# Kernel optimization log

Measured on AMD Instinct MI355X. Metric: run time of the kernel, lower is better.

## Reference

```python
import jax, jax.numpy as jnp
import numpy as np

DIM_MODEL = 512
DIM_HEAD = 64


def setup_inputs() -> dict:
    key = jax.random.key(0)
    ks = jax.random.split(key, 7)
    B, S = 4, 4096
    scale = 1.0 / np.sqrt(DIM_MODEL)
    x = jax.random.normal(ks[0], (B, S, DIM_MODEL), dtype=jnp.float32)
    # nn.Linear weights: stored as [out, in] in torch; we use [in, out] for x @ W
    Wq = jax.random.uniform(ks[1], (DIM_MODEL, DIM_HEAD), jnp.float32, -scale, scale)
    Wk = jax.random.uniform(ks[2], (DIM_MODEL, DIM_HEAD), jnp.float32, -scale, scale)
    Wv = jax.random.uniform(ks[3], (DIM_MODEL, DIM_HEAD), jnp.float32, -scale, scale)
    bq = jax.random.uniform(ks[4], (DIM_HEAD,), jnp.float32, -scale, scale)
    bk = jax.random.uniform(ks[5], (DIM_HEAD,), jnp.float32, -scale, scale)
    bv = jax.random.uniform(ks[6], (DIM_HEAD,), jnp.float32, -scale, scale)
    return {"x": x, "Wq": Wq, "bq": bq, "Wk": Wk, "bk": bk, "Wv": Wv, "bv": bv}


def reference(x, Wq, bq, Wk, bk, Wv, bv):
    # [q,k,v] = z @ U_qkv
    q = x @ Wq + bq  # [B, S, Dh]
    k = x @ Wk + bk
    v = x @ Wv + bv
    dot_scale = jnp.sqrt(jnp.asarray(DIM_HEAD, dtype=x.dtype))
    scores = jnp.einsum("bsd,btd->bst", q, k) / dot_scale  # [B, S, S]
    attn = jax.nn.softmax(scores, axis=-1)
    return jnp.einsum("bst,btd->bsd", attn, v)  # [B, S, Dh]
```

## Files before the change

### kernel.cpp

```cpp
#include <hip/hip_runtime.h>
#include <hip/hip_bf16.h>

typedef short short8 __attribute__((ext_vector_type(8)));
typedef float f32x4 __attribute__((ext_vector_type(4)));

#define MFMA16(a,b,c) __builtin_amdgcn_mfma_f32_16x16x32_bf16((a),(b),(c),0,0,0)

#define NROWS 16384
#define LOG2E 1.44269504088896340736f

#define OFF_Q  0u
#define OFF_K  (2u<<20)
#define OFF_V  (4u<<20)
#define OFF_W  (6u<<20)
#define OFF_O  ((6u<<20) + (1u<<18))

__device__ __forceinline__ unsigned short f2bf(float f){
    union { float f; unsigned u; } v; v.f = f;
    unsigned r = v.u + 0x7FFFu + ((v.u >> 16) & 1u);
    return (unsigned short)(r >> 16);
}
__device__ __forceinline__ unsigned pk2(float a, float b){
    union { __hip_bfloat162 h; unsigned u; } c;
    c.h = __float22bfloat162_rn(make_float2(a, b));
    return c.u;
}

union Frag {
    short8 s;
    unsigned short u[8];
    uint2 d2[2];
    uint4 q4;
};

__global__ __launch_bounds__(256) void wprep_kernel(
    const float* __restrict__ Wq, const float* __restrict__ Wk,
    const float* __restrict__ Wv, unsigned short* __restrict__ wfrag)
{
    int idx = blockIdx.x * 256 + threadIdx.x;
    int lane = idx & 63;
    int rest = idx >> 6;
    int kk = rest & 15;
    int nt = (rest >> 4) & 3;
    int w  = rest >> 6;
    const float* W = (w == 0) ? Wq : (w == 1) ? Wk : Wv;
    float scl = (w == 0) ? (0.125f * LOG2E) : 1.0f;
    int n = 16 * nt + (lane & 15);
    int g = lane >> 4;
    Frag o;
#pragma unroll
    for (int e = 0; e < 8; ++e) {
        int k = 32 * kk + 16 * (e >> 2) + 4 * g + (e & 3);
        o.u[e] = f2bf(W[k * 64 + n] * scl);
    }
    *(uint4*)(wfrag + (size_t)idx * 8) = o.q4;
}

#define LDW(WD, KK) do { \
    _Pragma("unroll") \
    for (int nt_ = 0; nt_ < 4; ++nt_) \
        WD[nt_].q4 = wf[((size_t)(nt_ * 16 + (KK))) * 64 + lane]; \
    } while (0)

#define DOK(WC, KK) do { \
    Frag xf_; \
    xf_.d2[0] = *(const uint2*)&xs[l15][32 * (KK) + 4 * g]; \
    xf_.d2[1] = *(const uint2*)&xs[l15][32 * (KK) + 16 + 4 * g]; \
    if (w == 2) { \
        _Pragma("unroll") \
        for (int nt_ = 0; nt_ < 4; ++nt_) acc[nt_] = MFMA16(xf_.s, WC[nt_].s, acc[nt_]); \
    } else { \
        _Pragma("unroll") \
        for (int nt_ = 0; nt_ < 4; ++nt_) acc[nt_] = MFMA16(WC[nt_].s, xf_.s, acc[nt_]); \
    } } while (0)

__global__ __launch_bounds__(192) void qkv_kernel(
    const float* __restrict__ x,
    const float* __restrict__ bq, const float* __restrict__ bk,
    const float* __restrict__ bv,
    const unsigned short* __restrict__ wfrag,
    unsigned short* __restrict__ qfrag,
    unsigned short* __restrict__ kfrag,
    unsigned short* __restrict__ vfrag)
{
    __shared__ unsigned short xs[16][520];
    const int tid = threadIdx.x;
    const int lane = tid & 63;
    const int w = tid >> 6;
    const int l15 = lane & 15, g = lane >> 4;
    const int rg = blockIdx.x;
    const float* xbase = x + (size_t)rg * 16 * 512;

    for (int i = tid; i < 2048; i += 192) {
        float4 v = *(const float4*)(xbase + i * 4);
        int r_ = i >> 7;
        int c_ = (i & 127) * 4;
        *(uint2*)&xs[r_][c_] = make_uint2(pk2(v.x, v.y), pk2(v.z, v.w));
    }
    __syncthreads();

    f32x4 acc[4];
#pragma unroll
    for (int nt = 0; nt < 4; ++nt) acc[nt] = (f32x4){0.f,0.f,0.f,0.f};

    const uint4* wf = (const uint4*)wfrag + (size_t)w * 4096;

    Frag wA[4], wB[4];
    LDW(wA, 0);
#pragma unroll
    for (int kp = 0; kp < 8; ++kp) {
        LDW(wB, 2 * kp + 1);
        __builtin_amdgcn_sched_barrier(0);
        DOK(wA, 2 * kp);
        if (2 * kp + 2 < 16) LDW(wA, 2 * kp + 2);
        __builtin_amdgcn_sched_barrier(0);
        DOK(wB, 2 * kp + 1);
    }

    const int b   = rg >> 8;
    const int rgb = rg & 255;
    const int tc  = rgb >> 2;
    const int c   = rgb & 3;

    if (w == 0) {
#pragma unroll
        for (int nt = 0; nt < 4; ++nt) {
            float4 bb = *(const float4*)(bq + 16 * nt + 4 * g);
            const float bs = 0.125f * LOG2E;
            float q0 = acc[nt][0] + bb.x * bs;
            float q1 = acc[nt][1] + bb.y * bs;
            float q2 = acc[nt][2] + bb.z * bs;
            float q3 = acc[nt][3] + bb.w * bs;
            int ks = nt >> 1, h = nt & 1;
            size_t qoff = ((size_t)(rg * 2 + ks) * 64 + lane) * 8 + h * 4;
            *(uint2*)(qfrag + qoff) = make_uint2(pk2(q0, q1), pk2(q2, q3));
        }
    } else if (w == 1) {
#pragma unroll
        for (int nt = 0; nt < 4; ++nt) {
            float4 bb = *(const float4*)(bk + 16 * nt + 4 * g);
            float k0 = acc[nt][0] + bb.x;
            float k1 = acc[nt][1] + bb.y;
            float k2 = acc[nt][2] + bb.z;
            float k3 = acc[nt][3] + bb.w;
            int ks = nt >> 1, h = nt & 1;
            size_t kfi = ((size_t)((b * 64 + tc) * 4 + c) * 2 + ks);
            size_t koff = (kfi * 64 + lane) * 8 + h * 4;
            *(uint2*)(kfrag + koff) = make_uint2(pk2(k0, k1), pk2(k2, k3));
        }
    } else {
        const int vks = c >> 1, vh = c & 1;
#pragma unroll
        for (int nt = 0; nt < 4; ++nt) {
            float bvv = bv[16 * nt + l15];
            float v0 = acc[nt][0] + bvv;
            float v1 = acc[nt][1] + bvv;
            float v2 = acc[nt][2] + bvv;
            float v3 = acc[nt][3] + bvv;
            size_t vfi = ((size_t)((b * 64 + tc) * 4 + nt) * 2 + vks);
            size_t voff = (vfi * 64 + lane) * 8 + vh * 4;
            *(uint2*)(vfrag + voff) = make_uint2(pk2(v0, v1), pk2(v2, v3));
        }
    }
}

#define LOADK(KD, CH) do { \
    const uint4* p_ = kb0 + (size_t)(CH) * 512; \
    _Pragma("unroll") \
    for (int c_ = 0; c_ < 4; ++c_) { \
        KD[c_][0].q4 = p_[(c_ * 2 + 0) * 64]; \
        KD[c_][1].q4 = p_[(c_ * 2 + 1) * 64]; \
    } } while (0)

#define LOADV(VD, CH) do { \
    const uint4* p_ = vb0 + (size_t)(CH) * 512; \
    _Pragma("unroll") \
    for (int c_ = 0; c_ < 4; ++c_) { \
        VD[c_][0].q4 = p_[(c_ * 2 + 0) * 64]; \
        VD[c_][1].q4 = p_[(c_ * 2 + 1) * 64]; \
    } } while (0)

#define BODY(KC, KN, CH, CHN) do { \
    Frag vC[4][2]; \
    LOADV(vC, CH); \
    LOADK(KN, CHN); \
    __builtin_amdgcn_sched_barrier(0); \
    _Pragma("unroll") \
    for (int M_ = 0; M_ < 4; ++M_) { \
        f32x4 sD[4]; \
        __builtin_amdgcn_s_setprio(1); \
        _Pragma("unroll") \
        for (int c_ = 0; c_ < 4; ++c_) { \
            f32x4 D = (f32x4){0.f,0.f,0.f,0.f}; \
            D = MFMA16(KC[c_][0].s, qf[M_][0].s, D); \
            D = MFMA16(KC[c_][1].s, qf[M_][1].s, D); \
            sD[c_] = D; \
        } \
        __builtin_amdgcn_s_setprio(0); \
        Frag pa0, pa1; \
        _Pragma("unroll") \
        for (int c_ = 0; c_ < 4; ++c_) { \
            float p0 = __builtin_exp2f(sD[c_][0]); \
            float p1 = __builtin_exp2f(sD[c_][1]); \
            float p2 = __builtin_exp2f(sD[c_][2]); \
            float p3 = __builtin_exp2f(sD[c_][3]); \
            uint2 pk_ = make_uint2(pk2(p0, p1), pk2(p2, p3)); \
            if (c_ < 2) pa0.d2[c_ & 1] = pk_; else pa1.d2[c_ & 1] = pk_; \
        } \
        __builtin_amdgcn_s_setprio(1); \
        lacc[M_] = MFMA16(pa0.s, ones_.s, lacc[M_]); \
        lacc[M_] = MFMA16(pa1.s, ones_.s, lacc[M_]); \
        _Pragma("unroll") \
        for (int dc_ = 0; dc_ < 4; ++dc_) { \
            acc[M_][dc_] = MFMA16(pa0.s, vC[dc_][0].s, acc[M_][dc_]); \
            acc[M_][dc_] = MFMA16(pa1.s, vC[dc_][1].s, acc[M_][dc_]); \
        } \
        __builtin_amdgcn_s_setprio(0); \
    } } while (0)

__global__ __launch_bounds__(256, 2) void attn_kernel(
    const unsigned short* __restrict__ qfrag,
    const unsigned short* __restrict__ kfrag,
    const unsigned short* __restrict__ vfrag,
    uint2* __restrict__ OpartU, float* __restrict__ lml,
    int CPS, int SBITS)
{
    const int tid = threadIdx.x;
    const int lane = tid & 63;
    const int w = tid >> 6;
    const int l15 = lane & 15, g = lane >> 4;
    const int split  = blockIdx.x & ((1 << SBITS) - 1);
    const int qblock = blockIdx.x >> SBITS;
    const int gw = qblock * 4 + w;
    const int b = gw >> 6;
    const int tcg0 = b * 64 + split * CPS;

    const uint4* qf4 = (const uint4*)qfrag;
    const uint4* kb0 = (const uint4*)kfrag + (size_t)tcg0 * 512 + lane;
    const uint4* vb0 = (const uint4*)vfrag + (size_t)tcg0 * 512 + lane;

    Frag qf[4][2];
#pragma unroll
    for (int M = 0; M < 4; ++M)
#pragma unroll
        for (int ks = 0; ks < 2; ++ks)
            qf[M][ks].q4 = qf4[((size_t)((gw * 4 + M) * 2 + ks)) * 64 + lane];

    Frag ones_;
    ones_.d2[0] = make_uint2(0x3F803F80u, 0x3F803F80u);
    ones_.d2[1] = make_uint2(0x3F803F80u, 0x3F803F80u);

    f32x4 acc[4][4], lacc[4];
#pragma unroll
    for (int M = 0; M < 4; ++M) {
        lacc[M] = (f32x4){0.f,0.f,0.f,0.f};
#pragma unroll
        for (int dc = 0; dc < 4; ++dc) acc[M][dc] = (f32x4){0.f,0.f,0.f,0.f};
    }

    Frag kA[4][2], kB[4][2];
    LOADK(kA, 0);

#pragma unroll 1
    for (int ch = 0; ch < CPS; ch += 2) {
        int c1 = (ch + 1 < CPS) ? (ch + 1) : ch;
        int c2 = (ch + 2 < CPS) ? (ch + 2) : ch;
        BODY(kA, kB, ch, c1);
        BODY(kB, kA, c1, c2);
    }

#pragma unroll
    for (int M = 0; M < 4; ++M) {
#pragma unroll
        for (int dc = 0; dc < 4; ++dc)
            OpartU[((size_t)(split * 256 + gw) * 16 + M * 4 + dc) * 64 + lane] =
                make_uint2(pk2(acc[M][dc][0], acc[M][dc][1]),
                           pk2(acc[M][dc][2], acc[M][dc][3]));
        if (l15 == 0)
            *(f32x4*)(lml + (size_t)(split * 256 + gw) * 64 + M * 16 + 4 * g) = lacc[M];
    }
}

__global__ __launch_bounds__(256) void merge_kernel(
    const uint2* __restrict__ OpartU, const float* __restrict__ lml,
    float* __restrict__ out, int S)
{
    int gid = blockIdx.x * 256 + threadIdx.x;
    int lane = gid & 63;
    int dc = (gid >> 6) & 3;
    int M  = (gid >> 8) & 3;
    int gw = gid >> 10;
    int l15 = lane & 15, g = lane >> 4;

    float o0 = 0.f, o1 = 0.f, o2 = 0.f, o3 = 0.f;
    float L0 = 0.f, L1 = 0.f, L2 = 0.f, L3 = 0.f;
    for (int s = 0; s < S; ++s) {
        uint2 pv = OpartU[((size_t)(s * 256 + gw) * 16 + M * 4 + dc) * 64 + lane];
        float4 lv = *(const float4*)(lml + (size_t)(s * 256 + gw) * 64 + M * 16 + 4 * g);
        o0 += __uint_as_float(pv.x << 16);
        o1 += __uint_as_float(pv.x & 0xFFFF0000u);
        o2 += __uint_as_float(pv.y << 16);
        o3 += __uint_as_float(pv.y & 0xFFFF0000u);
        L0 += lv.x; L1 += lv.y; L2 += lv.z; L3 += lv.w;
    }
    size_t row = (size_t)gw * 64 + M * 16 + 4 * g;
    int col = 16 * dc + l15;
    out[(row + 0) * 64 + col] = o0 / L0;
    out[(row + 1) * 64 + col] = o1 / L1;
    out[(row + 2) * 64 + col] = o2 / L2;
    out[(row + 3) * 64 + col] = o3 / L3;
}

extern "C" void kernel_launch(void* const* d_in, const int* in_sizes, int n_in,
                              void* d_out, int out_size, void* d_ws, size_t ws_size,
                              hipStream_t stream) {
    (void)in_sizes; (void)n_in; (void)out_size;
    const float* x  = (const float*)d_in[0];
    const float* Wq = (const float*)d_in[1];
    const float* bq = (const float*)d_in[2];
    const float* Wk = (const float*)d_in[3];
    const float* bk = (const float*)d_in[4];
    const float* Wv = (const float*)d_in[5];
    const float* bv = (const float*)d_in[6];
    float* out = (float*)d_out;

    char* ws = (char*)d_ws;
    unsigned short* qfrag = (unsigned short*)(ws + OFF_Q);
    unsigned short* kfrag = (unsigned short*)(ws + OFF_K);
    unsigned short* vfrag = (unsigned short*)(ws + OFF_V);
    unsigned short* wfrag = (unsigned short*)(ws + OFF_W);

    const size_t oneO = (size_t)256 * 16 * 64 * 8;
    const size_t oneL = (size_t)256 * 64 * 4;
    int S = 8, SBITS = 3;
    if (ws_size < (size_t)OFF_O + 8 * (oneO + oneL)) { S = 4; SBITS = 2; }
    if (ws_size < (size_t)OFF_O + 4 * (oneO + oneL)) { S = 2; SBITS = 1; }
    uint2* OpartU = (uint2*)(ws + OFF_O);
    float* lml    = (float*)(ws + OFF_O + (size_t)S * oneO);
    int CPS = 64 / S;

    hipLaunchKernelGGL(wprep_kernel, dim3(48), dim3(256), 0, stream,
                       Wq, Wk, Wv, wfrag);
    hipLaunchKernelGGL(qkv_kernel, dim3(1024), dim3(192), 0, stream,
                       x, bq, bk, bv, wfrag, qfrag, kfrag, vfrag);
    hipLaunchKernelGGL(attn_kernel, dim3(64 * S), dim3(256), 0, stream,
                       qfrag, kfrag, vfrag, OpartU, lml, CPS, SBITS);
    hipLaunchKernelGGL(merge_kernel, dim3(1024), dim3(256), 0, stream,
                       OpartU, lml, out, S);
}
```

Before: 59.17 us.

## Fuse split-K merge into attention kernel via shared-memory atomic reduction

The attention kernel now runs 8 waves per block, one per key-chunk split, all for the same 64-query group. Their partial outputs and row sums are combined with shared-memory atomics, and the normalized result is written straight to the output. This removes the bf16 partial-output round trip through global memory and the separate merge kernel launch. In exchange there are LDS atomic contention, two block barriers, a larger block size that may limit occupancy, a fixed split of 8 and a remapped block-to-query order.

```diff
diff --git a/kernel.cpp b/kernel.cpp
--- a/kernel.cpp
+++ b/kernel.cpp
@@ -13,7 +13,6 @@
 #define OFF_K  (2u<<20)
 #define OFF_V  (4u<<20)
 #define OFF_W  (6u<<20)
-#define OFF_O  ((6u<<20) + (1u<<18))
 
 __device__ __forceinline__ unsigned short f2bf(float f){
     union { float f; unsigned u; } v; v.f = f;
@@ -218,22 +217,25 @@
         __builtin_amdgcn_s_setprio(0); \
     } } while (0)
 
-__global__ __launch_bounds__(256, 2) void attn_kernel(
+__global__ __launch_bounds__(512, 2) void attn_kernel(
     const unsigned short* __restrict__ qfrag,
     const unsigned short* __restrict__ kfrag,
     const unsigned short* __restrict__ vfrag,
-    uint2* __restrict__ OpartU, float* __restrict__ lml,
-    int CPS, int SBITS)
+    float* __restrict__ out)
 {
+    __shared__ float Osh[64][65];
+    __shared__ float lsh[64];
     const int tid = threadIdx.x;
     const int lane = tid & 63;
     const int w = tid >> 6;
     const int l15 = lane & 15, g = lane >> 4;
-    const int split  = blockIdx.x & ((1 << SBITS) - 1);
-    const int qblock = blockIdx.x >> SBITS;
-    const int gw = qblock * 4 + w;
+    const int bid = blockIdx.x;
+    const int gw = ((bid & 7) << 5) | (bid >> 3);
     const int b = gw >> 6;
-    const int tcg0 = b * 64 + split * CPS;
+    const int tcg0 = b * 64 + w * 8;
+
+    for (int i = tid; i < 64 * 65; i += 512) (&Osh[0][0])[i] = 0.f;
+    if (tid < 64) lsh[tid] = 0.f;
 
     const uint4* qf4 = (const uint4*)qfrag;
     const uint4* kb0 = (const uint4*)kfrag + (size_t)tcg0 * 512 + lane;
@@ -262,59 +264,40 @@
     LOADK(kA, 0);
 
 #pragma unroll 1
-    for (int ch = 0; ch < CPS; ch += 2) {
-        int c1 = (ch + 1 < CPS) ? (ch + 1) : ch;
-        int c2 = (ch + 2 < CPS) ? (ch + 2) : ch;
+    for (int ch = 0; ch < 8; ch += 2) {
+        int c1 = ch + 1;
+        int c2 = (ch + 2 < 8) ? (ch + 2) : c1;
         BODY(kA, kB, ch, c1);
         BODY(kB, kA, c1, c2);
     }
 
+    __syncthreads();
 #pragma unroll
     for (int M = 0; M < 4; ++M) {
 #pragma unroll
         for (int dc = 0; dc < 4; ++dc)
-            OpartU[((size_t)(split * 256 + gw) * 16 + M * 4 + dc) * 64 + lane] =
-                make_uint2(pk2(acc[M][dc][0], acc[M][dc][1]),
-                           pk2(acc[M][dc][2], acc[M][dc][3]));
-        if (l15 == 0)
-            *(f32x4*)(lml + (size_t)(split * 256 + gw) * 64 + M * 16 + 4 * g) = lacc[M];
-    }
-}
-
-__global__ __launch_bounds__(256) void merge_kernel(
-    const uint2* __restrict__ OpartU, const float* __restrict__ lml,
-    float* __restrict__ out, int S)
-{
-    int gid = blockIdx.x * 256 + threadIdx.x;
-    int lane = gid & 63;
-    int dc = (gid >> 6) & 3;
-    int M  = (gid >> 8) & 3;
-    int gw = gid >> 10;
-    int l15 = lane & 15, g = lane >> 4;
-
-    float o0 = 0.f, o1 = 0.f, o2 = 0.f, o3 = 0.f;
-    float L0 = 0.f, L1 = 0.f, L2 = 0.f, L3 = 0.f;
-    for (int s = 0; s < S; ++s) {
-        uint2 pv = OpartU[((size_t)(s * 256 + gw) * 16 + M * 4 + dc) * 64 + lane];
-        float4 lv = *(const float4*)(lml + (size_t)(s * 256 + gw) * 64 + M * 16 + 4 * g);
-        o0 += __uint_as_float(pv.x << 16);
-        o1 += __uint_as_float(pv.x & 0xFFFF0000u);
-        o2 += __uint_as_float(pv.y << 16);
-        o3 += __uint_as_float(pv.y & 0xFFFF0000u);
-        L0 += lv.x; L1 += lv.y; L2 += lv.z; L3 += lv.w;
-    }
-    size_t row = (size_t)gw * 64 + M * 16 + 4 * g;
-    int col = 16 * dc + l15;
-    out[(row + 0) * 64 + col] = o0 / L0;
-    out[(row + 1) * 64 + col] = o1 / L1;
-    out[(row + 2) * 64 + col] = o2 / L2;
-    out[(row + 3) * 64 + col] = o3 / L3;
+#pragma unroll
+            for (int r = 0; r < 4; ++r)
+                atomicAdd(&Osh[16 * M + 4 * g + r][16 * dc + l15], acc[M][dc][r]);
+        if (l15 == 0) {
+#pragma unroll
+            for (int r = 0; r < 4; ++r)
+                atomicAdd(&lsh[16 * M + 4 * g + r], lacc[M][r]);
+        }
+    }
+    __syncthreads();
+
+    float* outb = out + (size_t)gw * 64 * 64;
+    for (int i = tid; i < 4096; i += 512) {
+        int row = i >> 6, col = i & 63;
+        outb[i] = Osh[row][col] / lsh[row];
+    }
 }
 
 extern "C" void kernel_launch(void* const* d_in, const int* in_sizes, int n_in,
                               void* d_out, int out_size, void* d_ws, size_t ws_size,
                               hipStream_t stream) {
-    (void)in_sizes; (void)n_in; (void)out_size;
+    (void)in_sizes; (void)n_in; (void)out_size; (void)ws_size;
     const float* x  = (const float*)d_in[0];
     const float* Wq = (const float*)d_in[1];
     const float* bq = (const float*)d_in[2];
@@ -330,21 +313,10 @@
     unsigned short* vfrag = (unsigned short*)(ws + OFF_V);
     unsigned short* wfrag = (unsigned short*)(ws + OFF_W);
 
-    const size_t oneO = (size_t)256 * 16 * 64 * 8;
-    const size_t oneL = (size_t)256 * 64 * 4;
-    int S = 8, SBITS = 3;
-    if (ws_size < (size_t)OFF_O + 8 * (oneO + oneL)) { S = 4; SBITS = 2; }
-    if (ws_size < (size_t)OFF_O + 4 * (oneO + oneL)) { S = 2; SBITS = 1; }
-    uint2* OpartU = (uint2*)(ws + OFF_O);
-    float* lml    = (float*)(ws + OFF_O + (size_t)S * oneO);
-    int CPS = 64 / S;
-
     hipLaunchKernelGGL(wprep_kernel, dim3(48), dim3(256), 0, stream,
                        Wq, Wk, Wv, wfrag);
     hipLaunchKernelGGL(qkv_kernel, dim3(1024), dim3(192), 0, stream,
                        x, bq, bk, bv, wfrag, qfrag, kfrag, vfrag);
-    hipLaunchKernelGGL(attn_kernel, dim3(64 * S), dim3(256), 0, stream,
-                       qfrag, kfrag, vfrag, OpartU, lml, CPS, SBITS);
-    hipLaunchKernelGGL(merge_kernel, dim3(1024), dim3(256), 0, stream,
-                       OpartU, lml, out, S);
-}
+    hipLaunchKernelGGL(attn_kernel, dim3(256), dim3(512), 0, stream,
+                       qfrag, kfrag, vfrag, out);
+}
```

After: 91.97 us. 1.55x slower.

## Stage K/V chunks into shared LDS via async global_load_lds double buffering

Applied to the files above, without the earlier changes.

Instead of each wave loading its own K and V fragments from global memory into registers, the four waves of a block cooperatively copy each K/V chunk into a double-buffered LDS tile with global_load_lds, then read the fragments from LDS. This removes the four-fold redundant global/L2 traffic across waves sharing the same batch and frees registers used for K/V prefetch. In exchange it adds LDS reads per MFMA group and a block-wide barrier per chunk. Correctness of the async copy relies on the barrier covering the in-flight global_load_lds, with no explicit vmcnt wait.

```diff
diff --git a/kernel.cpp b/kernel.cpp
--- a/kernel.cpp
+++ b/kernel.cpp
@@ -164,60 +164,6 @@
     }
 }
 
-#define LOADK(KD, CH) do { \
-    const uint4* p_ = kb0 + (size_t)(CH) * 512; \
-    _Pragma("unroll") \
-    for (int c_ = 0; c_ < 4; ++c_) { \
-        KD[c_][0].q4 = p_[(c_ * 2 + 0) * 64]; \
-        KD[c_][1].q4 = p_[(c_ * 2 + 1) * 64]; \
-    } } while (0)
-
-#define LOADV(VD, CH) do { \
-    const uint4* p_ = vb0 + (size_t)(CH) * 512; \
-    _Pragma("unroll") \
-    for (int c_ = 0; c_ < 4; ++c_) { \
-        VD[c_][0].q4 = p_[(c_ * 2 + 0) * 64]; \
-        VD[c_][1].q4 = p_[(c_ * 2 + 1) * 64]; \
-    } } while (0)
-
-#define BODY(KC, KN, CH, CHN) do { \
-    Frag vC[4][2]; \
-    LOADV(vC, CH); \
-    LOADK(KN, CHN); \
-    __builtin_amdgcn_sched_barrier(0); \
-    _Pragma("unroll") \
-    for (int M_ = 0; M_ < 4; ++M_) { \
-        f32x4 sD[4]; \
-        __builtin_amdgcn_s_setprio(1); \
-        _Pragma("unroll") \
-        for (int c_ = 0; c_ < 4; ++c_) { \
-            f32x4 D = (f32x4){0.f,0.f,0.f,0.f}; \
-            D = MFMA16(KC[c_][0].s, qf[M_][0].s, D); \
-            D = MFMA16(KC[c_][1].s, qf[M_][1].s, D); \
-            sD[c_] = D; \
-        } \
-        __builtin_amdgcn_s_setprio(0); \
-        Frag pa0, pa1; \
-        _Pragma("unroll") \
-        for (int c_ = 0; c_ < 4; ++c_) { \
-            float p0 = __builtin_exp2f(sD[c_][0]); \
-            float p1 = __builtin_exp2f(sD[c_][1]); \
-            float p2 = __builtin_exp2f(sD[c_][2]); \
-            float p3 = __builtin_exp2f(sD[c_][3]); \
-            uint2 pk_ = make_uint2(pk2(p0, p1), pk2(p2, p3)); \
-            if (c_ < 2) pa0.d2[c_ & 1] = pk_; else pa1.d2[c_ & 1] = pk_; \
-        } \
-        __builtin_amdgcn_s_setprio(1); \
-        lacc[M_] = MFMA16(pa0.s, ones_.s, lacc[M_]); \
-        lacc[M_] = MFMA16(pa1.s, ones_.s, lacc[M_]); \
-        _Pragma("unroll") \
-        for (int dc_ = 0; dc_ < 4; ++dc_) { \
-            acc[M_][dc_] = MFMA16(pa0.s, vC[dc_][0].s, acc[M_][dc_]); \
-            acc[M_][dc_] = MFMA16(pa1.s, vC[dc_][1].s, acc[M_][dc_]); \
-        } \
-        __builtin_amdgcn_s_setprio(0); \
-    } } while (0)
-
 __global__ __launch_bounds__(256, 2) void attn_kernel(
     const unsigned short* __restrict__ qfrag,
     const unsigned short* __restrict__ kfrag,
@@ -225,6 +171,7 @@
     uint2* __restrict__ OpartU, float* __restrict__ lml,
     int CPS, int SBITS)
 {
+    __shared__ unsigned short lds[2][16][64][8];
     const int tid = threadIdx.x;
     const int lane = tid & 63;
     const int w = tid >> 6;
@@ -236,8 +183,20 @@
     const int tcg0 = b * 64 + split * CPS;
 
     const uint4* qf4 = (const uint4*)qfrag;
-    const uint4* kb0 = (const uint4*)kfrag + (size_t)tcg0 * 512 + lane;
-    const uint4* vb0 = (const uint4*)vfrag + (size_t)tcg0 * 512 + lane;
+
+    auto stage = [&](int ch, int buf) {
+#pragma unroll
+        for (int i = 0; i < 4; ++i) {
+            int f = w * 4 + i;
+            const unsigned short* src = (f < 8)
+                ? (kfrag + (((size_t)(tcg0 + ch) * 8 + f) * 64 + lane) * 8)
+                : (vfrag + (((size_t)(tcg0 + ch) * 8 + (f - 8)) * 64 + lane) * 8);
+            __builtin_amdgcn_global_load_lds(
+                (const __attribute__((address_space(1))) unsigned int*)src,
+                (__attribute__((address_space(3))) unsigned int*)&lds[buf][f][0][0],
+                16, 0, 0);
+        }
+    };
 
     Frag qf[4][2];
 #pragma unroll
@@ -258,15 +217,59 @@
         for (int dc = 0; dc < 4; ++dc) acc[M][dc] = (f32x4){0.f,0.f,0.f,0.f};
     }
 
-    Frag kA[4][2], kB[4][2];
-    LOADK(kA, 0);
+    stage(0, 0);
+    __syncthreads();
+    int cur = 0;
 
 #pragma unroll 1
-    for (int ch = 0; ch < CPS; ch += 2) {
-        int c1 = (ch + 1 < CPS) ? (ch + 1) : ch;
-        int c2 = (ch + 2 < CPS) ? (ch + 2) : ch;
-        BODY(kA, kB, ch, c1);
-        BODY(kB, kA, c1, c2);
+    for (int ch = 0; ch < CPS; ++ch) {
+        if (ch + 1 < CPS) stage(ch + 1, cur ^ 1);
+
+        Frag kf[4][2];
+#pragma unroll
+        for (int c = 0; c < 4; ++c)
+#pragma unroll
+            for (int ks = 0; ks < 2; ++ks)
+                kf[c][ks].q4 = *(const uint4*)&lds[cur][c * 2 + ks][lane][0];
+
+#pragma unroll
+        for (int M = 0; M < 4; ++M) {
+            f32x4 sD[4];
+            __builtin_amdgcn_s_setprio(1);
+#pragma unroll
+            for (int c = 0; c < 4; ++c) {
+                f32x4 D = (f32x4){0.f,0.f,0.f,0.f};
+                D = MFMA16(kf[c][0].s, qf[M][0].s, D);
+                D = MFMA16(kf[c][1].s, qf[M][1].s, D);
+                sD[c] = D;
+            }
+            __builtin_amdgcn_s_setprio(0);
+            Frag pa0, pa1;
+#pragma unroll
+            for (int c = 0; c < 4; ++c) {
+                float p0 = __builtin_exp2f(sD[c][0]);
+                float p1 = __builtin_exp2f(sD[c][1]);
+                float p2 = __builtin_exp2f(sD[c][2]);
+                float p3 = __builtin_exp2f(sD[c][3]);
+                uint2 pk_ = make_uint2(pk2(p0, p1), pk2(p2, p3));
+                if (c < 2) pa0.d2[c & 1] = pk_; else pa1.d2[c & 1] = pk_;
+            }
+            __builtin_amdgcn_s_setprio(1);
+            lacc[M] = MFMA16(pa0.s, ones_.s, lacc[M]);
+            lacc[M] = MFMA16(pa1.s, ones_.s, lacc[M]);
+#pragma unroll
+            for (int dc = 0; dc < 4; ++dc) {
+                Frag vf0, vf1;
+                vf0.q4 = *(const uint4*)&lds[cur][8 + dc * 2 + 0][lane][0];
+                vf1.q4 = *(const uint4*)&lds[cur][8 + dc * 2 + 1][lane][0];
+                acc[M][dc] = MFMA16(pa0.s, vf0.s, acc[M][dc]);
+                acc[M][dc] = MFMA16(pa1.s, vf1.s, acc[M][dc]);
+            }
+            __builtin_amdgcn_s_setprio(0);
+        }
+
+        __syncthreads();
+        cur ^= 1;
     }
 
 #pragma unroll
```

After: 62.22 us. 1.05x slower.
